# Kernel tuning notes

Hardware: AMD Instinct MI355X
Metric: run time of the kernel (lower is better)

## Reference

```python
import jax, jax.numpy as jnp
import numpy as np

D_MODEL = 1024
NUM_HEADS = 16
HEAD_DIM = D_MODEL // NUM_HEADS
MASK_FUTURE = False
NEG_INF = -1.0e9


def setup_inputs() -> dict:
    key = jax.random.key(0)
    ks = jax.random.split(key, 8)
    B, L = 2, 2048
    q = jax.random.normal(ks[0], (B, L, D_MODEL), dtype=jnp.float32)
    k = jax.random.normal(ks[1], (B, L, D_MODEL), dtype=jnp.float32)
    v = jax.random.normal(ks[2], (B, L, D_MODEL), dtype=jnp.float32)
    attention_mask = jnp.ones((B, L), dtype=jnp.int32)
    s = 1.0 / np.sqrt(D_MODEL)
    Wq = jax.random.normal(ks[3], (D_MODEL, D_MODEL), dtype=jnp.float32) * s
    Wk = jax.random.normal(ks[4], (D_MODEL, D_MODEL), dtype=jnp.float32) * s
    Wv = jax.random.normal(ks[5], (D_MODEL, D_MODEL), dtype=jnp.float32) * s
    Wo = jax.random.normal(ks[6], (D_MODEL, D_MODEL), dtype=jnp.float32) * s
    return {"q": q, "k": k, "v": v, "attention_mask": attention_mask,
            "Wq": Wq, "Wk": Wk, "Wv": Wv, "Wo": Wo}


def _split_heads(x):
    B, L, _ = x.shape
    return x.reshape(B, L, NUM_HEADS, HEAD_DIM).transpose(0, 2, 1, 3)  # [B,H,L,Hd]


def reference(q, k, v, attention_mask, Wq, Wk, Wv, Wo):
    B, Lq, _ = q.shape
    Lk = k.shape[1]
    Q = _split_heads(q @ Wq.T)
    K = _split_heads(k @ Wk.T)
    V = _split_heads(v @ Wv.T)
    scale = HEAD_DIM ** 0.5  # per-head D in original Attention
    scores = jnp.einsum('bhqd,bhkd->bhqk', Q, K) / scale
    mask = (attention_mask == 0)[:, None, None, :]  # [B,1,1,Lk]
    scores = jnp.where(mask, NEG_INF, scores)
    if MASK_FUTURE:
        fut = jnp.triu(jnp.ones((Lq, Lk), dtype=bool), k=1)
        scores = jnp.where(fut[None, None], NEG_INF, scores)
    attn = jax.nn.softmax(scores, axis=-1)
    out = jnp.einsum('bhqk,bhkd->bhqd', attn, V)
    out = out.transpose(0, 2, 1, 3).reshape(B, Lq, D_MODEL)
    return out @ Wo.T
```

## Files before the change

kernel.cpp:

```cpp
#include <hip/hip_runtime.h>


#define D_MODEL 1024
#define NH 16
#define HD 64
#define BATCH 2
#define SEQ 2048
#define MROWS (BATCH*SEQ)

typedef unsigned short u16;
typedef __bf16 bf16x8 __attribute__((ext_vector_type(8)));
typedef float f32x4 __attribute__((ext_vector_type(4)));

__device__ __forceinline__ u16 f2bf(float f){
    __bf16 h = (__bf16)f;
    return __builtin_bit_cast(u16, h);
}
__device__ __forceinline__ float fast_exp2(float x){ return __builtin_amdgcn_exp2f(x); }

__device__ __forceinline__ void stage16(const void* g, void* l){
#if __has_builtin(__builtin_amdgcn_global_load_lds)
    __builtin_amdgcn_global_load_lds(
        (__attribute__((address_space(1))) void*)(unsigned long long)(g),
        (__attribute__((address_space(3))) void*)(unsigned int)(unsigned long long)(l),
        16, 0, 0);
#else
    *(uint4*)l = *(const uint4*)g;
#endif
}

__device__ __forceinline__ int detect_f32_block(const u16* q, int tid){
    __shared__ int flag;
    if (tid < 64){
        unsigned e = (q[2*tid]>>7)&0xFFu;
        bool hit = (e>=115u)&&(e<=132u);
        unsigned long long m = __ballot(hit);
        if (tid==0) flag = (__popcll(m) < 32) ? 1 : 0;
    }
    __syncthreads();
    return flag;
}

__global__ __launch_bounds__(256)
void convert_all(const u16* __restrict__ q, const u16* __restrict__ k,
                 const u16* __restrict__ v, const u16* __restrict__ Wq,
                 const u16* __restrict__ Wk, const u16* __restrict__ Wv,
                 const u16* __restrict__ Wo, u16* __restrict__ dst)
{
    int isf32 = detect_f32_block(q, threadIdx.x);
    int bid = blockIdx.x;
    const u16* src; int lb;
    if      (bid < 4096)  { src=q;  lb=bid; }
    else if (bid < 8192)  { src=k;  lb=bid-4096; }
    else if (bid < 12288) { src=v;  lb=bid-8192; }
    else if (bid < 13312) { src=Wq; lb=bid-12288; }
    else if (bid < 14336) { src=Wk; lb=bid-13312; }
    else if (bid < 15360) { src=Wv; lb=bid-14336; }
    else                  { src=Wo; lb=bid-15360; }
    size_t so = (size_t)lb*1024 + threadIdx.x*4;
    size_t dofs = (size_t)bid*1024 + threadIdx.x*4;
    if (isf32){
        float4 x = *(const float4*)((const float*)src + so);
        ushort4 o; o.x=f2bf(x.x); o.y=f2bf(x.y); o.z=f2bf(x.z); o.w=f2bf(x.w);
        *(ushort4*)(dst+dofs) = o;
    } else {
        *(ushort4*)(dst+dofs) = *(const ushort4*)(src+so);
    }
}

__global__ __launch_bounds__(256)
void gemm_qkv(const u16* __restrict__ qb, const u16* __restrict__ kb,
              const u16* __restrict__ vb, const u16* __restrict__ Wqb,
              const u16* __restrict__ Wkb, const u16* __restrict__ Wvb,
              u16* __restrict__ Qh, u16* __restrict__ Kh, u16* __restrict__ Vt)
{
    const int K = 1024;
    __shared__ __align__(16) u16 lA[128*32];
    __shared__ __align__(16) u16 lB[128*32];
    const int z = blockIdx.z;
    const u16* A  = (z==0)? qb  : (z==1)? kb  : vb;
    const u16* Bt = (z==0)? Wqb : (z==1)? Wkb : Wvb;

    const int tid  = threadIdx.x;
    const int wid  = tid>>6, lane = tid&63;
    const int quad = lane>>4, l16 = lane&15;
    const int wm = (wid>>1)*64, wn = (wid&1)*64;
    const int row0 = blockIdx.y*128, col0 = blockIdx.x*128;

    f32x4 acc[4][4];
    #pragma unroll
    for (int i=0;i<4;i++)
        #pragma unroll
        for (int j=0;j<4;j++) acc[i][j] = (f32x4){0.f,0.f,0.f,0.f};

    for (int k0=0; k0<K; k0+=32){
        #pragma unroll
        for (int s=0;s<2;s++){
            int c = tid + s*256;
            int r = c>>2, cc = (c&3)*8;
            stage16(&A [(size_t)(row0+r)*K + k0 + cc], &lA[c*8]);
            stage16(&Bt[(size_t)(col0+r)*K + k0 + cc], &lB[c*8]);
        }
        __syncthreads();
        bf16x8 af[4], bfr[4];
        #pragma unroll
        for (int mi=0;mi<4;mi++) af[mi]  = *(const bf16x8*)&lA[(wm+mi*16+l16)*32 + quad*8];
        #pragma unroll
        for (int ni=0;ni<4;ni++) bfr[ni] = *(const bf16x8*)&lB[(wn+ni*16+l16)*32 + quad*8];
        #pragma unroll
        for (int mi=0;mi<4;mi++)
            #pragma unroll
            for (int ni=0;ni<4;ni++)
                acc[mi][ni] = __builtin_amdgcn_mfma_f32_16x16x32_bf16(af[mi], bfr[ni], acc[mi][ni], 0,0,0);
        __syncthreads();
    }

    u16* Csh = (z==0)? Qh : Kh;
    #pragma unroll
    for (int mi=0;mi<4;mi++){
        #pragma unroll
        for (int ni=0;ni<4;ni++){
            int col = col0 + wn + ni*16 + l16;
            #pragma unroll
            for (int r=0;r<4;r++){
                int row = row0 + wm + mi*16 + quad*4 + r;
                u16 o = f2bf(acc[mi][ni][r]);
                int b = row>>11, i = row&2047, h = col>>6, d = col&63;
                if (z<2) Csh[((((size_t)(b*NH+h))*SEQ + i)<<6) + d] = o;
                else     Vt[((size_t)((b*NH+h)*HD + d))*SEQ + i] = o;
            }
        }
    }
}

__global__ __launch_bounds__(256)
void gemm_out(const u16* __restrict__ A, const u16* __restrict__ Bt,
              void* __restrict__ Cv, const u16* __restrict__ qref)
{
    const int K = 1024, N = 1024;
    int outf32 = detect_f32_block(qref, threadIdx.x);
    __shared__ __align__(16) u16 lA[64*32];
    __shared__ __align__(16) u16 lB[128*32];
    const int tid  = threadIdx.x;
    const int wid  = tid>>6, lane = tid&63;
    const int quad = lane>>4, l16 = lane&15;
    const int wm = (wid>>1)*32, wn = (wid&1)*64;
    const int row0 = blockIdx.y*64, col0 = blockIdx.x*128;

    f32x4 acc[2][4];
    #pragma unroll
    for (int i=0;i<2;i++)
        #pragma unroll
        for (int j=0;j<4;j++) acc[i][j] = (f32x4){0.f,0.f,0.f,0.f};

    for (int k0=0; k0<K; k0+=32){
        {
            int r = tid>>2, cc = (tid&3)*8;
            stage16(&A[(size_t)(row0+r)*K + k0 + cc], &lA[tid*8]);
        }
        #pragma unroll
        for (int s=0;s<2;s++){
            int c = tid + s*256;
            int r = c>>2, cc = (c&3)*8;
            stage16(&Bt[(size_t)(col0+r)*K + k0 + cc], &lB[c*8]);
        }
        __syncthreads();
        bf16x8 af[2], bfr[4];
        #pragma unroll
        for (int mi=0;mi<2;mi++) af[mi]  = *(const bf16x8*)&lA[(wm+mi*16+l16)*32 + quad*8];
        #pragma unroll
        for (int ni=0;ni<4;ni++) bfr[ni] = *(const bf16x8*)&lB[(wn+ni*16+l16)*32 + quad*8];
        #pragma unroll
        for (int mi=0;mi<2;mi++)
            #pragma unroll
            for (int ni=0;ni<4;ni++)
                acc[mi][ni] = __builtin_amdgcn_mfma_f32_16x16x32_bf16(af[mi], bfr[ni], acc[mi][ni], 0,0,0);
        __syncthreads();
    }

    #pragma unroll
    for (int mi=0;mi<2;mi++){
        #pragma unroll
        for (int ni=0;ni<4;ni++){
            int col = col0 + wn + ni*16 + l16;
            #pragma unroll
            for (int r=0;r<4;r++){
                int row = row0 + wm + mi*16 + quad*4 + r;
                float f = acc[mi][ni][r];
                if (outf32) ((float*)Cv)[(size_t)row*N + col] = f;
                else        ((u16*)Cv)[(size_t)row*N + col] = f2bf(f);
            }
        }
    }
}

#define KVT 4096
#define SW(row, c8) ((row)*64 + ((((c8) ^ ((row)&7)))*8))

__global__ __launch_bounds__(256)
void attn3(const u16* __restrict__ Qh, const u16* __restrict__ Kh,
           const u16* __restrict__ Vt, const int* __restrict__ mask,
           u16* __restrict__ ctx)
{
    __shared__ __align__(16) u16 lk[2*KVT];
    __shared__ __align__(16) u16 lv[2*KVT];
    __shared__ __align__(16) u16 lps[128*64];
    __shared__ unsigned mb[64];

    const int id = blockIdx.x;
    const int bh = (id&7)*4 + (id>>7);
    const int qb = (id>>3)&15;
    const int b = bh>>4, h = bh&15;
    const int i0 = qb*128;
    const int tid = threadIdx.x;
    const int wv = tid>>6, lane = tid&63;
    const int quad = lane>>4, l16 = lane&15;

    const u16* Qp  = Qh + ((size_t)bh*SEQ + i0)*HD;
    const u16* Kp  = Kh + (size_t)bh*SEQ*HD;
    const u16* Vtp = Vt + (size_t)bh*HD*SEQ;
    const int* mp  = mask + b*SEQ;

    #pragma unroll
    for (int s=0;s<4;s++){
        int c = tid + s*256;
        int r = c>>3, c8 = c&7;
        *(uint4*)&lps[SW(r,c8)] = *(const uint4*)&Qp[(size_t)r*HD + c8*8];
    }
    if (tid < 64){
        unsigned w = 0;
        #pragma unroll 8
        for (int i=0;i<32;i++) w |= (mp[tid*32+i] ? 1u:0u) << i;
        mb[tid] = w;
    }
    #pragma unroll
    for (int s=0;s<2;s++){
        int c = tid + s*256;
        int r = c>>3, c8 = c&7;
        *(uint4*)&lk[SW(r,c8)] = *(const uint4*)&Kp[(size_t)r*HD + c8*8];
        *(uint4*)&lv[SW(r,c8)] = *(const uint4*)&Vtp[(size_t)r*SEQ + c8*8];
    }
    __syncthreads();

    bf16x8 aq[2][2];
    #pragma unroll
    for (int mi=0;mi<2;mi++)
        #pragma unroll
        for (int kk=0;kk<2;kk++)
            aq[mi][kk] = *(const bf16x8*)&lps[SW(wv*32+mi*16+l16, kk*4+quad)];

    const int prow0 = wv*32;

    u16 onebits[8] = {0x3F80,0x3F80,0x3F80,0x3F80,0x3F80,0x3F80,0x3F80,0x3F80};
    bf16x8 bones = *(bf16x8*)onebits;

    f32x4 Oacc[2][4];
    f32x4 Lacc[2];
    #pragma unroll
    for (int mi=0;mi<2;mi++){
        Lacc[mi] = (f32x4){0.f,0.f,0.f,0.f};
        #pragma unroll
        for (int dn=0;dn<4;dn++) Oacc[mi][dn] = (f32x4){0.f,0.f,0.f,0.f};
    }

    const float SC = 0.125f * 1.44269504f;

    for (int t=0; t<32; t++){
        const int j0 = t*64;
        const u16* lkc = lk + (t&1)*KVT;
        const u16* lvc = lv + (t&1)*KVT;
        u16* lkn = lk + ((t&1)^1)*KVT;
        u16* lvn = lv + ((t&1)^1)*KVT;

        __syncthreads();

        uint4 gk[2], gv[2];
        if (t < 31){
            #pragma unroll
            for (int s=0;s<2;s++){
                int c = tid + s*256;
                int r = c>>3, c8 = c&7;
                gk[s] = *(const uint4*)&Kp[(size_t)(j0+64+r)*HD + c8*8];
                gv[s] = *(const uint4*)&Vtp[(size_t)r*SEQ + j0+64 + c8*8];
            }
        }

        f32x4 sfr[2][4];
        #pragma unroll
        for (int jn=0;jn<4;jn++){
            bf16x8 bk0 = *(const bf16x8*)&lkc[SW(jn*16+l16, quad)];
            bf16x8 bk1 = *(const bf16x8*)&lkc[SW(jn*16+l16, 4+quad)];
            #pragma unroll
            for (int mi=0;mi<2;mi++){
                f32x4 a0 = (f32x4){0.f,0.f,0.f,0.f};
                a0 = __builtin_amdgcn_mfma_f32_16x16x32_bf16(aq[mi][0], bk0, a0, 0,0,0);
                a0 = __builtin_amdgcn_mfma_f32_16x16x32_bf16(aq[mi][1], bk1, a0, 0,0,0);
                sfr[mi][jn] = a0;
            }
        }

        unsigned mw0 = mb[t*2], mw1 = mb[t*2+1];
        #pragma unroll
        for (int jn=0;jn<4;jn++){
            unsigned mw = (jn<2)? mw0 : mw1;
            int sh = (jn&1)*16 + l16;
            float bias = ((mw>>sh)&1u) ? 0.f : -1.5e9f;
            int c8 = jn*2 + (l16>>3), cb = l16&7;
            #pragma unroll
            for (int mi=0;mi<2;mi++){
                #pragma unroll
                for (int r=0;r<4;r++){
                    float p = fast_exp2(sfr[mi][jn][r]*SC + bias);
                    lps[SW(prow0+mi*16+quad*4+r, c8) + cb] = f2bf(p);
                }
            }
        }
        bf16x8 ap[2][2];
        #pragma unroll
        for (int mi=0;mi<2;mi++)
            #pragma unroll
            for (int kk=0;kk<2;kk++)
                ap[mi][kk] = *(const bf16x8*)&lps[SW(prow0+mi*16+l16, kk*4+quad)];

        #pragma unroll
        for (int dn=0;dn<4;dn++){
            #pragma unroll
            for (int kk=0;kk<2;kk++){
                bf16x8 bv = *(const bf16x8*)&lvc[SW(dn*16+l16, kk*4+quad)];
                #pragma unroll
                for (int mi=0;mi<2;mi++)
                    Oacc[mi][dn] = __builtin_amdgcn_mfma_f32_16x16x32_bf16(ap[mi][kk], bv, Oacc[mi][dn], 0,0,0);
            }
        }
        #pragma unroll
        for (int mi=0;mi<2;mi++)
            #pragma unroll
            for (int kk=0;kk<2;kk++)
                Lacc[mi] = __builtin_amdgcn_mfma_f32_16x16x32_bf16(ap[mi][kk], bones, Lacc[mi], 0,0,0);

        if (t < 31){
            #pragma unroll
            for (int s=0;s<2;s++){
                int c = tid + s*256;
                int r = c>>3, c8 = c&7;
                *(uint4*)&lkn[SW(r,c8)] = gk[s];
                *(uint4*)&lvn[SW(r,c8)] = gv[s];
            }
        }
    }

    #pragma unroll
    for (int mi=0;mi<2;mi++){
        f32x4 rl;
        #pragma unroll
        for (int r=0;r<4;r++) rl[r] = 1.0f / Lacc[mi][r];
        #pragma unroll
        for (int dn=0;dn<4;dn++){
            int col = h*HD + dn*16 + l16;
            #pragma unroll
            for (int r=0;r<4;r++){
                int i = i0 + wv*32 + mi*16 + quad*4 + r;
                ctx[((size_t)(b*SEQ + i))*D_MODEL + col] = f2bf(Oacc[mi][dn][r]*rl[r]);
            }
        }
    }
}

extern "C" void kernel_launch(void* const* d_in, const int* in_sizes, int n_in,
                              void* d_out, int out_size, void* d_ws, size_t ws_size,
                              hipStream_t stream)
{
    (void)in_sizes; (void)n_in; (void)out_size; (void)ws_size;
    const u16* q    = (const u16*)d_in[0];
    const u16* k    = (const u16*)d_in[1];
    const u16* v    = (const u16*)d_in[2];
    const int* mask = (const int*)d_in[3];
    const u16* Wq   = (const u16*)d_in[4];
    const u16* Wk   = (const u16*)d_in[5];
    const u16* Wv   = (const u16*)d_in[6];
    const u16* Wo   = (const u16*)d_in[7];

    const size_t TEN = (size_t)MROWS * D_MODEL;
    const size_t WEL = (size_t)D_MODEL * D_MODEL;
    u16* qb  = (u16*)d_ws;
    u16* kb  = qb + TEN;
    u16* vb  = kb + TEN;
    u16* Wqb = vb + TEN;
    u16* Wkb = Wqb + WEL;
    u16* Wvb = Wkb + WEL;
    u16* Wob = Wvb + WEL;
    u16* Qh  = Wob + WEL;
    u16* Kh  = Qh + TEN;
    u16* Vtr = Kh + TEN;
    u16* ctx = Vtr + TEN;

    dim3 bb(256);
    convert_all<<<dim3(16384), bb, 0, stream>>>(q,k,v,Wq,Wk,Wv,Wo, qb);
    gemm_qkv<<<dim3(8,32,3), bb, 0, stream>>>(qb,kb,vb, Wqb,Wkb,Wvb, Qh,Kh,Vtr);
    attn3<<<dim3(512), bb, 0, stream>>>(Qh, Kh, Vtr, mask, ctx);
    gemm_out<<<dim3(8,64), bb, 0, stream>>>(ctx, Wob, d_out, q);
}
```

Baseline: 241.4 us.

## Keep attention probabilities in registers using 32x32 MFMA transposed scores

Rewrites the attention inner loop to compute S^T with 32x32x16 MFMAs so the exp'd probabilities land directly in the register layout needed as the A operand of the PV MFMA. This removes the LDS round-trip for P and the Q staging buffer. The softmax scale is folded into the Q projection epilogue, and the mask is applied only when a tile contains masked keys. V fragments are gathered with two 8-byte LDS reads per operand, which may raise LDS instruction count and bank pressure; scheduling priority is also raised around the MFMA section.

After: 261.5 us. 8.3% more time.

```diff
diff --git a/kernel.cpp b/kernel.cpp
--- a/kernel.cpp
+++ b/kernel.cpp
@@ -11,6 +11,7 @@
 typedef unsigned short u16;
 typedef __bf16 bf16x8 __attribute__((ext_vector_type(8)));
 typedef float f32x4 __attribute__((ext_vector_type(4)));
+typedef float f32x16 __attribute__((ext_vector_type(16)));
 
 __device__ __forceinline__ u16 f2bf(float f){
     __bf16 h = (__bf16)f;
@@ -115,6 +116,7 @@
         __syncthreads();
     }
 
+    const float qsc = (z==0) ? 0.18033688011112042f : 1.0f;
     u16* Csh = (z==0)? Qh : Kh;
     #pragma unroll
     for (int mi=0;mi<4;mi++){
@@ -124,7 +126,7 @@
             #pragma unroll
             for (int r=0;r<4;r++){
                 int row = row0 + wm + mi*16 + quad*4 + r;
-                u16 o = f2bf(acc[mi][ni][r]);
+                u16 o = f2bf(acc[mi][ni][r]*qsc);
                 int b = row>>11, i = row&2047, h = col>>6, d = col&63;
                 if (z<2) Csh[((((size_t)(b*NH+h))*SEQ + i)<<6) + d] = o;
                 else     Vt[((size_t)((b*NH+h)*HD + d))*SEQ + i] = o;
@@ -197,6 +199,14 @@
 #define KVT 4096
 #define SW(row, c8) ((row)*64 + ((((c8) ^ ((row)&7)))*8))
 
+__device__ __forceinline__ bf16x8 ldv_nat(const u16* lvc, int row, int chunk2, int hi){
+    uint2 lo = *(const uint2*)&lvc[SW(row, chunk2)   + 4*hi];
+    uint2 hj = *(const uint2*)&lvc[SW(row, chunk2+1) + 4*hi];
+    union { uint4 u; bf16x8 v; } r;
+    r.u.x = lo.x; r.u.y = lo.y; r.u.z = hj.x; r.u.w = hj.y;
+    return r.v;
+}
+
 __global__ __launch_bounds__(256)
 void attn3(const u16* __restrict__ Qh, const u16* __restrict__ Kh,
            const u16* __restrict__ Vt, const int* __restrict__ mask,
@@ -204,7 +214,6 @@
 {
     __shared__ __align__(16) u16 lk[2*KVT];
     __shared__ __align__(16) u16 lv[2*KVT];
-    __shared__ __align__(16) u16 lps[128*64];
     __shared__ unsigned mb[64];
 
     const int id = blockIdx.x;
@@ -214,19 +223,12 @@
     const int i0 = qb*128;
     const int tid = threadIdx.x;
     const int wv = tid>>6, lane = tid&63;
-    const int quad = lane>>4, l16 = lane&15;
-
-    const u16* Qp  = Qh + ((size_t)bh*SEQ + i0)*HD;
+    const int l31 = lane&31, hi = lane>>5;
+
     const u16* Kp  = Kh + (size_t)bh*SEQ*HD;
     const u16* Vtp = Vt + (size_t)bh*HD*SEQ;
     const int* mp  = mask + b*SEQ;
 
-    #pragma unroll
-    for (int s=0;s<4;s++){
-        int c = tid + s*256;
-        int r = c>>3, c8 = c&7;
-        *(uint4*)&lps[SW(r,c8)] = *(const uint4*)&Qp[(size_t)r*HD + c8*8];
-    }
     if (tid < 64){
         unsigned w = 0;
         #pragma unroll 8
@@ -240,30 +242,19 @@
         *(uint4*)&lk[SW(r,c8)] = *(const uint4*)&Kp[(size_t)r*HD + c8*8];
         *(uint4*)&lv[SW(r,c8)] = *(const uint4*)&Vtp[(size_t)r*SEQ + c8*8];
     }
-    __syncthreads();
-
-    bf16x8 aq[2][2];
-    #pragma unroll
-    for (int mi=0;mi<2;mi++)
-        #pragma unroll
-        for (int kk=0;kk<2;kk++)
-            aq[mi][kk] = *(const bf16x8*)&lps[SW(wv*32+mi*16+l16, kk*4+quad)];
-
-    const int prow0 = wv*32;
-
-    u16 onebits[8] = {0x3F80,0x3F80,0x3F80,0x3F80,0x3F80,0x3F80,0x3F80,0x3F80};
-    bf16x8 bones = *(bf16x8*)onebits;
-
-    f32x4 Oacc[2][4];
-    f32x4 Lacc[2];
-    #pragma unroll
-    for (int mi=0;mi<2;mi++){
-        Lacc[mi] = (f32x4){0.f,0.f,0.f,0.f};
-        #pragma unroll
-        for (int dn=0;dn<4;dn++) Oacc[mi][dn] = (f32x4){0.f,0.f,0.f,0.f};
-    }
-
-    const float SC = 0.125f * 1.44269504f;
+
+    const u16* Qrow = Qh + ((size_t)bh*SEQ + i0 + wv*32 + l31)*HD;
+    bf16x8 aq[4];
+    #pragma unroll
+    for (int kk=0;kk<4;kk++) aq[kk] = *(const bf16x8*)&Qrow[kk*16 + hi*8];
+
+    bf16x8 bones;
+    #pragma unroll
+    for (int j=0;j<8;j++) ((u16*)&bones)[j] = 0x3F80;
+
+    f32x16 Oacc[2], Lacc;
+    #pragma unroll
+    for (int r=0;r<16;r++){ Oacc[0][r]=0.f; Oacc[1][r]=0.f; Lacc[r]=0.f; }
 
     for (int t=0; t<32; t++){
         const int j0 = t*64;
@@ -285,58 +276,54 @@
             }
         }
 
-        f32x4 sfr[2][4];
-        #pragma unroll
-        for (int jn=0;jn<4;jn++){
-            bf16x8 bk0 = *(const bf16x8*)&lkc[SW(jn*16+l16, quad)];
-            bf16x8 bk1 = *(const bf16x8*)&lkc[SW(jn*16+l16, 4+quad)];
-            #pragma unroll
-            for (int mi=0;mi<2;mi++){
-                f32x4 a0 = (f32x4){0.f,0.f,0.f,0.f};
-                a0 = __builtin_amdgcn_mfma_f32_16x16x32_bf16(aq[mi][0], bk0, a0, 0,0,0);
-                a0 = __builtin_amdgcn_mfma_f32_16x16x32_bf16(aq[mi][1], bk1, a0, 0,0,0);
-                sfr[mi][jn] = a0;
-            }
-        }
-
-        unsigned mw0 = mb[t*2], mw1 = mb[t*2+1];
-        #pragma unroll
-        for (int jn=0;jn<4;jn++){
-            unsigned mw = (jn<2)? mw0 : mw1;
-            int sh = (jn&1)*16 + l16;
-            float bias = ((mw>>sh)&1u) ? 0.f : -1.5e9f;
-            int c8 = jn*2 + (l16>>3), cb = l16&7;
-            #pragma unroll
-            for (int mi=0;mi<2;mi++){
+        __builtin_amdgcn_s_setprio(1);
+        #pragma unroll
+        for (int jt=0; jt<2; ++jt){
+            f32x16 sfr;
+            #pragma unroll
+            for (int r=0;r<16;r++) sfr[r]=0.f;
+            #pragma unroll
+            for (int kk=0;kk<4;kk++){
+                bf16x8 ak = *(const bf16x8*)&lkc[SW(jt*32+l31, 2*kk+hi)];
+                sfr = __builtin_amdgcn_mfma_f32_32x32x16_bf16(ak, aq[kk], sfr, 0,0,0);
+            }
+
+            unsigned mw = mb[2*t+jt];
+            if ((unsigned)__builtin_amdgcn_readfirstlane((int)mw) != 0xFFFFFFFFu){
+                unsigned ms = mw >> (hi*4);
                 #pragma unroll
-                for (int r=0;r<4;r++){
-                    float p = fast_exp2(sfr[mi][jn][r]*SC + bias);
-                    lps[SW(prow0+mi*16+quad*4+r, c8) + cb] = f2bf(p);
+                for (int r=0;r<16;r++){
+                    int kb = (r&3)+8*(r>>2);
+                    if (!((ms>>kb)&1u)) sfr[r] = -1.0e9f;
                 }
             }
-        }
-        bf16x8 ap[2][2];
-        #pragma unroll
-        for (int mi=0;mi<2;mi++)
-            #pragma unroll
-            for (int kk=0;kk<2;kk++)
-                ap[mi][kk] = *(const bf16x8*)&lps[SW(prow0+mi*16+l16, kk*4+quad)];
-
-        #pragma unroll
-        for (int dn=0;dn<4;dn++){
-            #pragma unroll
-            for (int kk=0;kk<2;kk++){
-                bf16x8 bv = *(const bf16x8*)&lvc[SW(dn*16+l16, kk*4+quad)];
-                #pragma unroll
-                for (int mi=0;mi<2;mi++)
-                    Oacc[mi][dn] = __builtin_amdgcn_mfma_f32_16x16x32_bf16(ap[mi][kk], bv, Oacc[mi][dn], 0,0,0);
-            }
-        }
-        #pragma unroll
-        for (int mi=0;mi<2;mi++)
-            #pragma unroll
-            for (int kk=0;kk<2;kk++)
-                Lacc[mi] = __builtin_amdgcn_mfma_f32_16x16x32_bf16(ap[mi][kk], bones, Lacc[mi], 0,0,0);
+
+            unsigned cc[8];
+            #pragma unroll
+            for (int d=0; d<8; ++d){
+                float p0 = fast_exp2(sfr[2*d]);
+                float p1 = fast_exp2(sfr[2*d+1]);
+                cc[d] = (unsigned)f2bf(p0) | ((unsigned)f2bf(p1)<<16);
+            }
+            bf16x8 pa0, pa1;
+            ((unsigned*)&pa0)[0]=cc[0]; ((unsigned*)&pa0)[1]=cc[1];
+            ((unsigned*)&pa0)[2]=cc[2]; ((unsigned*)&pa0)[3]=cc[3];
+            ((unsigned*)&pa1)[0]=cc[4]; ((unsigned*)&pa1)[1]=cc[5];
+            ((unsigned*)&pa1)[2]=cc[6]; ((unsigned*)&pa1)[3]=cc[7];
+
+            Lacc = __builtin_amdgcn_mfma_f32_32x32x16_bf16(pa0, bones, Lacc, 0,0,0);
+            Lacc = __builtin_amdgcn_mfma_f32_32x32x16_bf16(pa1, bones, Lacc, 0,0,0);
+
+            #pragma unroll
+            for (int dn=0; dn<2; ++dn){
+                int vr = dn*32 + l31;
+                bf16x8 bv0 = ldv_nat(lvc, vr, jt*4,   hi);
+                bf16x8 bv1 = ldv_nat(lvc, vr, jt*4+2, hi);
+                Oacc[dn] = __builtin_amdgcn_mfma_f32_32x32x16_bf16(pa0, bv0, Oacc[dn], 0,0,0);
+                Oacc[dn] = __builtin_amdgcn_mfma_f32_32x32x16_bf16(pa1, bv1, Oacc[dn], 0,0,0);
+            }
+        }
+        __builtin_amdgcn_s_setprio(0);
 
         if (t < 31){
             #pragma unroll
@@ -349,19 +336,16 @@
         }
     }
 
-    #pragma unroll
-    for (int mi=0;mi<2;mi++){
-        f32x4 rl;
-        #pragma unroll
-        for (int r=0;r<4;r++) rl[r] = 1.0f / Lacc[mi][r];
-        #pragma unroll
-        for (int dn=0;dn<4;dn++){
-            int col = h*HD + dn*16 + l16;
-            #pragma unroll
-            for (int r=0;r<4;r++){
-                int i = i0 + wv*32 + mi*16 + quad*4 + r;
-                ctx[((size_t)(b*SEQ + i))*D_MODEL + col] = f2bf(Oacc[mi][dn][r]*rl[r]);
-            }
+    float rc[16];
+    #pragma unroll
+    for (int r=0;r<16;r++) rc[r] = 1.0f / Lacc[r];
+    #pragma unroll
+    for (int dn=0; dn<2; ++dn){
+        int col = h*HD + dn*32 + l31;
+        #pragma unroll
+        for (int r=0;r<16;r++){
+            int row = i0 + wv*32 + (r&3) + 8*(r>>2) + 4*hi;
+            ctx[((size_t)(b*SEQ+row))*D_MODEL + col] = f2bf(Oacc[dn][r] * rc[r]);
         }
     }
 }
```
